# Kernel tuning notes

Hardware: AMD Instinct MI355X
Metric: run time of the kernel (lower is better)

Reference implementation:

```python
import jax, jax.numpy as jnp
import numpy as np
import math

H = 4096        # hidden_size
INNER = 4096    # hidden_inner_size = NH * HD
NH = 32         # num_heads
HD = 128        # head_dim
SEQ = 4096      # prefill sequence length (batch = 1, as asserted in source)
BLOCK = 256     # chunk size of the lightning-attention recurrence
NUM_LAYERS = 32
LAYER_IDX = 0
EPS = 1e-5


def _build_slopes(n):
    # Faithful port of MiniMaxText01LinearAttention._build_slope_tensor
    def p2(m):
        start = 2 ** (-2 ** (-(math.log2(m) - 3)))
        return [start * start ** i for i in range(m)]
    if math.log2(n).is_integer():
        s = p2(n)
    else:
        c = 2 ** math.floor(math.log2(n))
        s = p2(c) + p2(2 * c)[0::2][: n - c]
    return np.array(s, dtype=np.float32)


def setup_inputs() -> dict:
    key = jax.random.key(0)
    ks = jax.random.split(key, 4)
    x = jax.random.normal(ks[0], (SEQ, H), jnp.float32)
    w_qkv = jax.random.normal(ks[1], (3 * INNER, H), jnp.float32) * 0.02
    w_gate = jax.random.normal(ks[2], (INNER, H), jnp.float32) * 0.02
    w_out = jax.random.normal(ks[3], (H, INNER), jnp.float32) * 0.02
    norm_weight = jnp.ones((INNER,), jnp.float32)
    kv_cache = jnp.zeros((NH, HD, HD), jnp.float32)
    slope = jnp.asarray(_build_slopes(NH) * (1.0 - LAYER_IDX / (NUM_LAYERS - 1) + 1e-5))
    return dict(x=x, w_qkv=w_qkv, w_gate=w_gate, w_out=w_out,
                norm_weight=norm_weight, kv_cache=kv_cache, slope=slope)


def _lightning_attn(q, k, v, slope, kv0, block):
    # q,k,v: [h, n, d]; slope: [h]; kv0: [h, d, d] running KV state
    h, n, d = q.shape
    nb = n // block
    idx = jnp.arange(block, dtype=jnp.float32) + 1.0  # 1..block, as in lightning_attn2
    s = slope[:, None, None]                                   # [h,1,1]
    q_dec = jnp.exp(-s * idx[None, :, None])                   # [h,m,1]
    k_dec = jnp.exp(-s * (block - idx)[None, :, None])         # [h,m,1]
    diff = idx[:, None] - idx[None, :]                         # [m,m]
    diag_dec = jnp.where(diff[None] >= 0, jnp.exp(-s * diff[None]), 0.0)  # [h,m,m]
    blk_dec = jnp.exp(-slope * block)[:, None, None]           # [h,1,1]

    # [nb, h, m, d] blocks for scan
    qb = q.reshape(h, nb, block, d).transpose(1, 0, 2, 3)
    kb = k.reshape(h, nb, block, d).transpose(1, 0, 2, 3)
    vb = v.reshape(h, nb, block, d).transpose(1, 0, 2, 3)

    def step(kv, blk):
        qi, ki, vi = blk
        o_inter = jnp.einsum('hmd,hde->hme', qi * q_dec, kv)
        qk = jnp.einsum('hmd,hnd->hmn', qi, ki) * diag_dec
        o_intra = jnp.einsum('hmn,hne->hme', qk, vi)
        kv_new = blk_dec * kv + jnp.einsum('hmd,hme->hde', ki * k_dec, vi)
        return kv_new, o_inter + o_intra

    kv_final, ob = jax.lax.scan(step, kv0, (qb, kb, vb))
    out = ob.transpose(1, 0, 2, 3).reshape(h, n, d)
    return out, kv_final


def reference(x, w_qkv, w_gate, w_out, norm_weight, kv_cache, slope):
    # qkv projection + silu (fp32, as in source)
    qkv = jax.nn.silu((x @ w_qkv.T).astype(jnp.float32))       # [n, 3*inner]
    qkv = qkv.reshape(SEQ, NH, 3 * HD)                         # per-head interleaved q|k|v
    q, k, v = jnp.split(qkv, 3, axis=-1)
    q, k, v = (t.transpose(1, 0, 2) for t in (q, k, v))        # [h, n, d]
    attn, _ = _lightning_attn(q, k, v, slope.astype(jnp.float32), kv_cache, BLOCK)
    hidden = attn.transpose(1, 0, 2).reshape(SEQ, INNER)       # 'h n d -> n (h d)'
    # RMSNorm in fp32
    var = jnp.mean(hidden.astype(jnp.float32) ** 2, axis=-1, keepdims=True)
    normed = hidden * jax.lax.rsqrt(var + EPS) * norm_weight
    # gated output projection
    gate = jax.nn.sigmoid(x @ w_gate.T)
    out = (gate * normed) @ w_out.T
    return out
```

## Files before the change

kernel.cpp:

```cpp
#include <hip/hip_runtime.h>

typedef __bf16 bf16;
typedef __bf16 bf16x8 __attribute__((ext_vector_type(8)));
typedef __bf16 bf16x4 __attribute__((ext_vector_type(4)));
typedef float floatx4 __attribute__((ext_vector_type(4)));

#define MFMA16(a, b, c) __builtin_amdgcn_mfma_f32_16x16x32_bf16(a, b, c, 0, 0, 0)

#define GLOAD_LDS16(g, l)                                          \
  __builtin_amdgcn_global_load_lds(                                \
      (const __attribute__((address_space(1))) void*)(g),          \
      (__attribute__((address_space(3))) void*)(l), 16, 0, 0)

#define BAR() __builtin_amdgcn_s_barrier()
#define SCHED0() __builtin_amdgcn_sched_barrier(0)
#define LGKM0()                                        \
  do {                                                 \
    asm volatile("s_waitcnt lgkmcnt(0)" ::: "memory"); \
    __builtin_amdgcn_sched_barrier(0);                 \
  } while (0)
#define VM6() asm volatile("s_waitcnt vmcnt(6)" ::: "memory")

#define MFMA_PHASE(HM, HN, BB)                                            \
  do {                                                                    \
    __builtin_amdgcn_s_setprio(1);                                        \
    _Pragma("unroll") for (int kk = 0; kk < 2; ++kk)                      \
        _Pragma("unroll") for (int mf = 0; mf < 4; ++mf)                  \
            _Pragma("unroll") for (int nf = 0; nf < 2; ++nf)              \
                acc[HM][HN][mf][nf] =                                     \
        MFMA16(af[kk][mf], BB[kk][nf], acc[HM][HN][mf][nf]);              \
    __builtin_amdgcn_s_setprio(0);                                        \
  } while (0)

__global__ __launch_bounds__(256) void cvt_bf16(const float* __restrict__ src,
                                                bf16* __restrict__ dst, long n) {
  const long i = ((long)blockIdx.x * 256 + threadIdx.x) * 8;
  if (i >= n) return;
  float4 a = *(const float4*)&src[i];
  float4 b = *(const float4*)&src[i + 4];
  bf16x8 o = {(bf16)a.x, (bf16)a.y, (bf16)a.z, (bf16)a.w,
              (bf16)b.x, (bf16)b.y, (bf16)b.z, (bf16)b.w};
  *(bf16x8*)&dst[i] = o;
}

template <int EPI>
__global__ __launch_bounds__(512, 2) void gemm256(const bf16* __restrict__ A,
                                                  const bf16* __restrict__ B,
                                                  void* __restrict__ Cv,
                                                  int N, int K) {
  __shared__ bf16 AS[2][256 * 64];
  __shared__ bf16 BS[2][256 * 64];
  const int tid = threadIdx.x;
  const int wave = tid >> 6, lane = tid & 63;
  const int quad = lane >> 4, l16 = lane & 15;
  const int wm = wave >> 2, wn = wave & 3;
  const int cswz = (l16 & 12) << 2;
  const int gc = ((lane & 7) * 8) ^
                 (((((wave & 1) << 1) | ((lane >> 5) & 1))) << 4);

  int wg = blockIdx.x;
  {
    const int nwg = gridDim.x;
    const int q = nwg >> 3, r = nwg & 7, xcd = wg & 7, idx = wg >> 3;
    wg = (xcd < r ? xcd * (q + 1) : r * (q + 1) + (xcd - r) * q) + idx;
  }
  const int nbn = N >> 8;
  const int bm = wg / nbn, bn = wg - bm * nbn;

  const bf16* gA = A + (long)(bm * 256) * K;
  const bf16* gB = B + (long)(bn * 256) * K;

  auto stA = [&](int buf, int h, int kt) {
#pragma unroll
    for (int j = 0; j < 2; ++j) {
      const int rb = h * 128 + j * 64 + wave * 8;
      GLOAD_LDS16(gA + (long)(rb + (lane >> 3)) * K + kt * 64 + gc,
                  &AS[buf][rb * 64]);
    }
  };
  auto stB = [&](int buf, int h, int kt) {
#pragma unroll
    for (int j = 0; j < 2; ++j) {
      const int rb = h * 128 + j * 64 + wave * 8;
      GLOAD_LDS16(gB + (long)(rb + (lane >> 3)) * K + kt * 64 + gc,
                  &BS[buf][rb * 64]);
    }
  };

  bf16x8 af[2][4], b0[2][2], b1[2][2];
  floatx4 acc[2][2][4][2] = {};

  auto rdA = [&](int buf, int hm) {
#pragma unroll
    for (int kk = 0; kk < 2; ++kk)
#pragma unroll
      for (int mf = 0; mf < 4; ++mf) {
        const int R = hm * 128 + wm * 64 + mf * 16 + l16;
        af[kk][mf] =
            *(const bf16x8*)&AS[buf][R * 64 + ((kk * 32 + quad * 8) ^ cswz)];
      }
  };
  auto rdB = [&](int buf, int hn, bf16x8 (&bb)[2][2]) {
#pragma unroll
    for (int kk = 0; kk < 2; ++kk)
#pragma unroll
      for (int nf = 0; nf < 2; ++nf) {
        const int R = hn * 128 + wn * 32 + nf * 16 + l16;
        bb[kk][nf] =
            *(const bf16x8*)&BS[buf][R * 64 + ((kk * 32 + quad * 8) ^ cswz)];
      }
  };

  const int NT = K >> 6;
  const int NI = NT >> 1;

  stA(0, 0, 0); stA(0, 1, 0); stB(0, 0, 0); stB(0, 1, 0);
  stA(1, 0, 1); stB(1, 0, 1); stB(1, 1, 1);
  VM6();
  BAR();

  for (int it = 0; it < NI; ++it) {
    const int t1 = 2 * it + 1;
    const int t2 = (2 * it + 2 < NT) ? 2 * it + 2 : NT - 1;
    const int t3 = (2 * it + 3 < NT) ? 2 * it + 3 : NT - 1;
    rdA(0, 0); rdB(0, 0, b0);
    stA(1, 1, t1);
    SCHED0(); BAR(); LGKM0();
    MFMA_PHASE(0, 0, b0);
    BAR();
    rdB(0, 1, b1);
    stA(0, 0, t2);
    SCHED0(); BAR(); LGKM0();
    MFMA_PHASE(0, 1, b1);
    BAR();
    rdA(0, 1);
    stB(0, 0, t2);
    SCHED0(); BAR(); LGKM0();
    MFMA_PHASE(1, 0, b0);
    BAR();
    stB(0, 1, t2);
    VM6(); SCHED0(); BAR(); SCHED0();
    MFMA_PHASE(1, 1, b1);
    BAR();
    rdA(1, 0); rdB(1, 0, b0);
    stA(0, 1, t2);
    SCHED0(); BAR(); LGKM0();
    MFMA_PHASE(0, 0, b0);
    BAR();
    rdB(1, 1, b1);
    stA(1, 0, t3);
    SCHED0(); BAR(); LGKM0();
    MFMA_PHASE(0, 1, b1);
    BAR();
    rdA(1, 1);
    stB(1, 0, t3);
    SCHED0(); BAR(); LGKM0();
    MFMA_PHASE(1, 0, b0);
    BAR();
    stB(1, 1, t3);
    VM6(); SCHED0(); BAR(); SCHED0();
    MFMA_PHASE(1, 1, b1);
    BAR();
  }

#pragma unroll
  for (int hm = 0; hm < 2; ++hm)
#pragma unroll
    for (int hn = 0; hn < 2; ++hn)
#pragma unroll
      for (int mf = 0; mf < 4; ++mf)
#pragma unroll
        for (int nf = 0; nf < 2; ++nf)
#pragma unroll
          for (int r = 0; r < 4; ++r) {
            const int row = bm * 256 + hm * 128 + wm * 64 + mf * 16 + quad * 4 + r;
            const int col = bn * 256 + hn * 128 + wn * 32 + nf * 16 + l16;
            const float v = acc[hm][hn][mf][nf][r];
            if constexpr (EPI == 0) {
              ((bf16*)Cv)[(long)row * N + col] = (bf16)(v / (1.f + __expf(-v)));
            } else if constexpr (EPI == 1) {
              ((bf16*)Cv)[(long)row * N + col] = (bf16)(1.f / (1.f + __expf(-v)));
            } else {
              ((float*)Cv)[(long)row * N + col] = v;
            }
          }
}

__global__ __launch_bounds__(256) void transpose_kv(const bf16* __restrict__ qkvb,
                                                    bf16* __restrict__ kT,
                                                    bf16* __restrict__ vT) {
  __shared__ bf16 tile[64][72];
  const int tid = threadIdx.x;
  const int t0 = blockIdx.x * 64;
  const int qz = blockIdx.y;
  const int h = blockIdx.z;
  const int srccol = h * 384 + 128 + (qz >> 1) * 128 + (qz & 1) * 64;
  const int row = tid >> 2, cb = (tid & 3) * 16;
#pragma unroll
  for (int i = 0; i < 2; ++i)
    *(bf16x8*)&tile[row][cb + i * 8] =
        *(const bf16x8*)&qkvb[(long)(t0 + row) * 12288 + srccol + cb + i * 8];
  __syncthreads();
  bf16* dst = (qz >= 2) ? vT : kT;
  const int ch = (qz & 1) * 64 + (tid >> 2);
#pragma unroll
  for (int i = 0; i < 2; ++i) {
    bf16x8 v;
#pragma unroll
    for (int j = 0; j < 8; ++j) v[j] = tile[cb + i * 8 + j][tid >> 2];
    *(bf16x8*)&dst[((long)h * 128 + ch) * 4096 + t0 + cb + i * 8] = v;
  }
}

__global__ __launch_bounds__(256) void kv_blocks(const bf16* __restrict__ kT,
                                                 const bf16* __restrict__ vT,
                                                 const float* __restrict__ slope,
                                                 float* __restrict__ MT) {
  __shared__ float kdec[256];
  const int tid = threadIdx.x;
  const int b = blockIdx.x, h = blockIdx.y;
  const float s = slope[h];
  if (tid < 256) kdec[tid] = __expf(-s * (float)(255 - tid));
  __syncthreads();
  const int wave = tid >> 6, lane = tid & 63;
  const int quad = lane >> 4, l16 = lane & 15;
  const int we = (wave & 1) * 64, wd = (wave >> 1) * 64;
  floatx4 acc[4][4] = {};
  for (int kc = 0; kc < 8; ++kc) {
    const int ioff = kc * 32 + quad * 8;
    bf16x8 af[4], bfr[4];
#pragma unroll
    for (int mt = 0; mt < 4; ++mt)
      af[mt] = *(const bf16x8*)&vT[((long)h * 128 + we + mt * 16 + l16) * 4096 +
                                   b * 256 + ioff];
#pragma unroll
    for (int nt = 0; nt < 4; ++nt) {
      bf16x8 k8 = *(const bf16x8*)&kT[((long)h * 128 + wd + nt * 16 + l16) * 4096 +
                                      b * 256 + ioff];
      bf16x8 kb;
#pragma unroll
      for (int j = 0; j < 8; ++j) kb[j] = (bf16)((float)k8[j] * kdec[ioff + j]);
      bfr[nt] = kb;
    }
#pragma unroll
    for (int mt = 0; mt < 4; ++mt)
#pragma unroll
      for (int nt = 0; nt < 4; ++nt)
        acc[mt][nt] = MFMA16(af[mt], bfr[nt], acc[mt][nt]);
  }
#pragma unroll
  for (int mt = 0; mt < 4; ++mt)
#pragma unroll
    for (int nt = 0; nt < 4; ++nt)
#pragma unroll
      for (int r = 0; r < 4; ++r) {
        const int e = we + mt * 16 + quad * 4 + r;
        const int d = wd + nt * 16 + l16;
        MT[(((long)h * 16 + b) * 128 + e) * 128 + d] = acc[mt][nt][r];
      }
}

__global__ __launch_bounds__(256) void kv_scan(const float* __restrict__ MT,
                                               const float* __restrict__ kvc,
                                               const float* __restrict__ slope,
                                               bf16* __restrict__ ST) {
  const long idx = (long)blockIdx.x * 256 + threadIdx.x;
  const int d = idx & 127;
  const int e = (int)((idx >> 7) & 127);
  const int h = (int)(idx >> 14);
  const float s = slope[h];
  const float bd = __expf(-s * 256.f);
  float kv = kvc[((long)h * 128 + d) * 128 + e];
#pragma unroll
  for (int b = 0; b < 16; ++b) {
    const long o = (((long)h * 16 + b) * 128 + e) * 128 + d;
    ST[o] = (bf16)kv;
    kv = bd * kv + MT[o];
  }
}

__global__ __launch_bounds__(512) void attn_out(const bf16* __restrict__ qkvb,
                                                const bf16* __restrict__ vT,
                                                const bf16* __restrict__ ST,
                                                const float* __restrict__ slope,
                                                float* __restrict__ hidden) {
  __shared__ float ddt[257];
  __shared__ bf16 sbuf[8][32][72];
  const int tid = threadIdx.x;
  const int b = blockIdx.x, h = blockIdx.y;
  const float s = slope[h];
  if (tid < 257) ddt[tid] = __expf(-s * (float)tid);
  __syncthreads();
  const int wave = tid >> 6, lane = tid & 63;
  const int quad = lane >> 4, l16 = lane & 15;
  const int iw = wave * 32;
  floatx4 oacc[2][8] = {};
  for (int jb = 0; jb < 4; ++jb) {
    floatx4 sacc[2][4] = {};
#pragma unroll
    for (int kc = 0; kc < 4; ++kc) {
      bf16x8 qf[2], kf[4];
#pragma unroll
      for (int mt = 0; mt < 2; ++mt)
        qf[mt] = *(const bf16x8*)&qkvb[(long)(b * 256 + iw + mt * 16 + l16) * 12288 +
                                       h * 384 + kc * 32 + quad * 8];
#pragma unroll
      for (int nt = 0; nt < 4; ++nt)
        kf[nt] = *(const bf16x8*)&qkvb[(long)(b * 256 + jb * 64 + nt * 16 + l16) * 12288 +
                                       h * 384 + 128 + kc * 32 + quad * 8];
#pragma unroll
      for (int mt = 0; mt < 2; ++mt)
#pragma unroll
        for (int nt = 0; nt < 4; ++nt)
          sacc[mt][nt] = MFMA16(qf[mt], kf[nt], sacc[mt][nt]);
    }
#pragma unroll
    for (int mt = 0; mt < 2; ++mt)
#pragma unroll
      for (int nt = 0; nt < 4; ++nt)
#pragma unroll
        for (int r = 0; r < 4; ++r) {
          const int i = iw + mt * 16 + quad * 4 + r;
          const int j = jb * 64 + nt * 16 + l16;
          const int diff = i - j;
          const float v = (diff >= 0) ? sacc[mt][nt][r] * ddt[diff] : 0.f;
          sbuf[wave][mt * 16 + quad * 4 + r][nt * 16 + l16] = (bf16)v;
        }
    __syncthreads();
#pragma unroll
    for (int kc2 = 0; kc2 < 2; ++kc2) {
      bf16x8 sf[2];
#pragma unroll
      for (int mt = 0; mt < 2; ++mt)
        sf[mt] = *(const bf16x8*)&sbuf[wave][mt * 16 + l16][kc2 * 32 + quad * 8];
#pragma unroll
      for (int et = 0; et < 8; ++et) {
        bf16x8 vf = *(const bf16x8*)&vT[((long)h * 128 + et * 16 + l16) * 4096 +
                                        b * 256 + jb * 64 + kc2 * 32 + quad * 8];
#pragma unroll
        for (int mt = 0; mt < 2; ++mt)
          oacc[mt][et] = MFMA16(sf[mt], vf, oacc[mt][et]);
      }
    }
    __syncthreads();
  }
#pragma unroll
  for (int kc = 0; kc < 4; ++kc) {
    bf16x8 qf[2];
#pragma unroll
    for (int mt = 0; mt < 2; ++mt) {
      bf16x8 q8 = *(const bf16x8*)&qkvb[(long)(b * 256 + iw + mt * 16 + l16) * 12288 +
                                        h * 384 + kc * 32 + quad * 8];
      const float qd = ddt[iw + mt * 16 + l16 + 1];
      bf16x8 qq;
#pragma unroll
      for (int j = 0; j < 8; ++j) qq[j] = (bf16)((float)q8[j] * qd);
      qf[mt] = qq;
    }
#pragma unroll
    for (int et = 0; et < 8; ++et) {
      bf16x8 kvf = *(const bf16x8*)&ST[(((long)h * 16 + b) * 128 + et * 16 + l16) * 128 +
                                       kc * 32 + quad * 8];
#pragma unroll
      for (int mt = 0; mt < 2; ++mt)
        oacc[mt][et] = MFMA16(qf[mt], kvf, oacc[mt][et]);
    }
  }
#pragma unroll
  for (int mt = 0; mt < 2; ++mt)
#pragma unroll
    for (int et = 0; et < 8; ++et)
#pragma unroll
      for (int r = 0; r < 4; ++r) {
        const int t = b * 256 + iw + mt * 16 + quad * 4 + r;
        const int e = et * 16 + l16;
        hidden[(long)t * 4096 + h * 128 + e] = oacc[mt][et][r];
      }
}

__global__ __launch_bounds__(256) void rms_gate(const float* __restrict__ hidden,
                                                const bf16* __restrict__ gateb,
                                                const float* __restrict__ nw,
                                                bf16* __restrict__ afinal) {
  const int t = blockIdx.x, tid = threadIdx.x;
  const float* rowp = hidden + (long)t * 4096;
  float ss = 0.f;
  float4 hv[4];
#pragma unroll
  for (int i = 0; i < 4; ++i) {
    hv[i] = ((const float4*)rowp)[tid + i * 256];
    ss += hv[i].x * hv[i].x + hv[i].y * hv[i].y + hv[i].z * hv[i].z + hv[i].w * hv[i].w;
  }
#pragma unroll
  for (int off = 32; off > 0; off >>= 1) ss += __shfl_down(ss, off);
  __shared__ float red[4];
  if ((tid & 63) == 0) red[tid >> 6] = ss;
  __syncthreads();
  const float tot = red[0] + red[1] + red[2] + red[3];
  const float rs = rsqrtf(tot * (1.f / 4096.f) + 1e-5f);
#pragma unroll
  for (int i = 0; i < 4; ++i) {
    const int c = (tid + i * 256) * 4;
    bf16x4 g = *(const bf16x4*)&gateb[(long)t * 4096 + c];
    float4 w = *(const float4*)&nw[c];
    bf16x4 o;
    o[0] = (bf16)(hv[i].x * rs * w.x * (float)g[0]);
    o[1] = (bf16)(hv[i].y * rs * w.y * (float)g[1]);
    o[2] = (bf16)(hv[i].z * rs * w.z * (float)g[2]);
    o[3] = (bf16)(hv[i].w * rs * w.w * (float)g[3]);
    *(bf16x4*)&afinal[(long)t * 4096 + c] = o;
  }
}

extern "C" void kernel_launch(void* const* d_in, const int* in_sizes, int n_in,
                              void* d_out, int out_size, void* d_ws, size_t ws_size,
                              hipStream_t stream) {
  (void)in_sizes; (void)n_in; (void)out_size;
  const float* x      = (const float*)d_in[0];
  const float* w_qkv  = (const float*)d_in[1];
  const float* w_gate = (const float*)d_in[2];
  const float* w_out  = (const float*)d_in[3];
  const float* nw     = (const float*)d_in[4];
  const float* kvc    = (const float*)d_in[5];
  const float* slope  = (const float*)d_in[6];
  float* out = (float*)d_out;

  const size_t MB = 1024 * 1024;
  char* base = (char*)d_ws;
  bf16* qkvb   = (bf16*)(base + 0 * MB);
  bf16* kT     = (bf16*)(base + 96 * MB);
  bf16* vT     = (bf16*)(base + 128 * MB);
  bf16* wob    = (bf16*)(base + 160 * MB);
  bf16* gateb  = (bf16*)(base + 192 * MB);
  bf16* xb     = (bf16*)(base + 224 * MB);
  bf16* afinal = (bf16*)(base + 224 * MB);
  bf16* wb     = (bf16*)(base + 256 * MB);
  float* MT    = (float*)(base + 256 * MB);
  bf16* ST     = (bf16*)(base + 288 * MB);
  float* hidden= (float*)(base + 304 * MB);
  if (ws_size < 384 * MB) return;

  const long nx = 4096L * 4096, nqkv = 12288L * 4096;
  cvt_bf16<<<dim3((int)(nx / 2048)), 256, 0, stream>>>(x, xb, nx);
  cvt_bf16<<<dim3((int)(nqkv / 2048)), 256, 0, stream>>>(w_qkv, wb, nqkv);
  cvt_bf16<<<dim3((int)(nx / 2048)), 256, 0, stream>>>(w_gate, wb + nqkv, nx);
  cvt_bf16<<<dim3((int)(nx / 2048)), 256, 0, stream>>>(w_out, wob, nx);
  gemm256<0><<<dim3(16 * 48), 512, 0, stream>>>(xb, wb, qkvb, 12288, 4096);
  gemm256<1><<<dim3(16 * 16), 512, 0, stream>>>(xb, wb + nqkv, gateb, 4096, 4096);
  transpose_kv<<<dim3(64, 4, 32), 256, 0, stream>>>(qkvb, kT, vT);
  kv_blocks<<<dim3(16, 32), 256, 0, stream>>>(kT, vT, slope, MT);
  kv_scan<<<dim3(2048), 256, 0, stream>>>(MT, kvc, slope, ST);
  attn_out<<<dim3(16, 32), 512, 0, stream>>>(qkvb, vT, ST, slope, hidden);
  rms_gate<<<dim3(4096), 256, 0, stream>>>(hidden, gateb, nw, afinal);
  gemm256<2><<<dim3(16 * 16), 512, 0, stream>>>(afinal, wob, out, 4096, 4096);
}
```

Before: 1.371 ms.

## Software-pipeline LDS fragment reads behind MFMAs with one barrier per window

Reworks the bf16 GEMM main loop into eight uniform windows. Each window issues one global-to-LDS stage, runs its MFMA block, then prefetches the LDS fragments needed by the next window before a single vmcnt wait and barrier. This removes the explicit lgkmcnt(0) wait and the second barrier that sat in front of every MFMA phase, so LDS read latency can hide behind matrix math. The B-fragment readers are split into fixed-half variants and the prologue is reordered to preload the first fragments. The risk is in the barrier and buffer reuse ordering: if it is wrong, LDS tiles get overwritten while still being read, and holding prefetched fragments raises register pressure.

After: 1.276 ms. 6.9% less time.

```diff
diff --git a/kernel.cpp b/kernel.cpp
--- a/kernel.cpp
+++ b/kernel.cpp
@@ -14,23 +14,7 @@
 
 #define BAR() __builtin_amdgcn_s_barrier()
 #define SCHED0() __builtin_amdgcn_sched_barrier(0)
-#define LGKM0()                                        \
-  do {                                                 \
-    asm volatile("s_waitcnt lgkmcnt(0)" ::: "memory"); \
-    __builtin_amdgcn_sched_barrier(0);                 \
-  } while (0)
 #define VM6() asm volatile("s_waitcnt vmcnt(6)" ::: "memory")
-
-#define MFMA_PHASE(HM, HN, BB)                                            \
-  do {                                                                    \
-    __builtin_amdgcn_s_setprio(1);                                        \
-    _Pragma("unroll") for (int kk = 0; kk < 2; ++kk)                      \
-        _Pragma("unroll") for (int mf = 0; mf < 4; ++mf)                  \
-            _Pragma("unroll") for (int nf = 0; nf < 2; ++nf)              \
-                acc[HM][HN][mf][nf] =                                     \
-        MFMA16(af[kk][mf], BB[kk][nf], acc[HM][HN][mf][nf]);              \
-    __builtin_amdgcn_s_setprio(0);                                        \
-  } while (0)
 
 __global__ __launch_bounds__(256) void cvt_bf16(const float* __restrict__ src,
                                                 bf16* __restrict__ dst, long n) {
@@ -90,7 +74,7 @@
   bf16x8 af[2][4], b0[2][2], b1[2][2];
   floatx4 acc[2][2][4][2] = {};
 
-  auto rdA = [&](int buf, int hm) {
+  auto rdAf = [&](int buf, int hm) {
 #pragma unroll
     for (int kk = 0; kk < 2; ++kk)
 #pragma unroll
@@ -100,67 +84,70 @@
             *(const bf16x8*)&AS[buf][R * 64 + ((kk * 32 + quad * 8) ^ cswz)];
       }
   };
-  auto rdB = [&](int buf, int hn, bf16x8 (&bb)[2][2]) {
+  auto rdB0 = [&](int buf) {
 #pragma unroll
     for (int kk = 0; kk < 2; ++kk)
 #pragma unroll
       for (int nf = 0; nf < 2; ++nf) {
-        const int R = hn * 128 + wn * 32 + nf * 16 + l16;
-        bb[kk][nf] =
+        const int R = wn * 32 + nf * 16 + l16;
+        b0[kk][nf] =
             *(const bf16x8*)&BS[buf][R * 64 + ((kk * 32 + quad * 8) ^ cswz)];
       }
   };
+  auto rdB1 = [&](int buf) {
+#pragma unroll
+    for (int kk = 0; kk < 2; ++kk)
+#pragma unroll
+      for (int nf = 0; nf < 2; ++nf) {
+        const int R = 128 + wn * 32 + nf * 16 + l16;
+        b1[kk][nf] =
+            *(const bf16x8*)&BS[buf][R * 64 + ((kk * 32 + quad * 8) ^ cswz)];
+      }
+  };
+
+#define MFMA_Q(HM, HN, BB)                                                \
+  do {                                                                    \
+    __builtin_amdgcn_s_setprio(1);                                        \
+    _Pragma("unroll") for (int kk = 0; kk < 2; ++kk)                      \
+        _Pragma("unroll") for (int mf = 0; mf < 4; ++mf)                  \
+            _Pragma("unroll") for (int nf = 0; nf < 2; ++nf)              \
+                acc[HM][HN][mf][nf] =                                     \
+        MFMA16(af[kk][mf], BB[kk][nf], acc[HM][HN][mf][nf]);              \
+    __builtin_amdgcn_s_setprio(0);                                        \
+  } while (0)
+
+#define WINDOW(STG, HM, HN, BB, RD) \
+  do {                              \
+    STG;                            \
+    MFMA_Q(HM, HN, BB);             \
+    SCHED0();                       \
+    RD;                             \
+    SCHED0();                       \
+    VM6();                          \
+    BAR();                          \
+  } while (0)
 
   const int NT = K >> 6;
   const int NI = NT >> 1;
 
-  stA(0, 0, 0); stA(0, 1, 0); stB(0, 0, 0); stB(0, 1, 0);
-  stA(1, 0, 1); stB(1, 0, 1); stB(1, 1, 1);
+  stB(0, 0, 0); stA(0, 0, 0); stB(0, 1, 0); stA(0, 1, 0);
+  stB(1, 0, 1); stA(1, 0, 1);
   VM6();
   BAR();
+  rdB0(0); rdAf(0, 0);
 
   for (int it = 0; it < NI; ++it) {
     const int t1 = 2 * it + 1;
     const int t2 = (2 * it + 2 < NT) ? 2 * it + 2 : NT - 1;
     const int t3 = (2 * it + 3 < NT) ? 2 * it + 3 : NT - 1;
-    rdA(0, 0); rdB(0, 0, b0);
-    stA(1, 1, t1);
-    SCHED0(); BAR(); LGKM0();
-    MFMA_PHASE(0, 0, b0);
-    BAR();
-    rdB(0, 1, b1);
-    stA(0, 0, t2);
-    SCHED0(); BAR(); LGKM0();
-    MFMA_PHASE(0, 1, b1);
-    BAR();
-    rdA(0, 1);
-    stB(0, 0, t2);
-    SCHED0(); BAR(); LGKM0();
-    MFMA_PHASE(1, 0, b0);
-    BAR();
-    stB(0, 1, t2);
-    VM6(); SCHED0(); BAR(); SCHED0();
-    MFMA_PHASE(1, 1, b1);
-    BAR();
-    rdA(1, 0); rdB(1, 0, b0);
-    stA(0, 1, t2);
-    SCHED0(); BAR(); LGKM0();
-    MFMA_PHASE(0, 0, b0);
-    BAR();
-    rdB(1, 1, b1);
-    stA(1, 0, t3);
-    SCHED0(); BAR(); LGKM0();
-    MFMA_PHASE(0, 1, b1);
-    BAR();
-    rdA(1, 1);
-    stB(1, 0, t3);
-    SCHED0(); BAR(); LGKM0();
-    MFMA_PHASE(1, 0, b0);
-    BAR();
-    stB(1, 1, t3);
-    VM6(); SCHED0(); BAR(); SCHED0();
-    MFMA_PHASE(1, 1, b1);
-    BAR();
+    WINDOW(stB(1, 1, t1), 0, 0, b0, rdB1(0));
+    WINDOW(stA(1, 1, t1), 0, 1, b1, rdAf(0, 1));
+    WINDOW(stB(0, 0, t2), 1, 0, b0, rdB0(1));
+    WINDOW(stA(0, 0, t2), 1, 1, b1, rdAf(1, 0));
+    WINDOW(stB(0, 1, t2), 0, 0, b0, rdB1(1));
+    WINDOW(stA(0, 1, t2), 0, 1, b1, rdAf(1, 1));
+    WINDOW(stB(1, 0, t3), 1, 0, b0, rdB0(0));
+    WINDOW(stA(1, 0, t3), 1, 1, b1, rdAf(0, 0));
   }
 
 #pragma unroll
@@ -184,6 +171,8 @@
               ((float*)Cv)[(long)row * N + col] = v;
             }
           }
+#undef MFMA_Q
+#undef WINDOW
 }
 
 __global__ __launch_bounds__(256) void transpose_kv(const bf16* __restrict__ qkvb,
```
